# Optimization experiments

Measured on AMD Instinct MI355X. Metric: run time of the kernel, lower is better.

Reference implementation:

```python
import jax, jax.numpy as jnp
import numpy as np

TEMP = 2.0   # distillation temperature
KL_W = 0.2   # kl loss weight


def setup_inputs() -> dict:
    key = jax.random.key(0)
    ks = jax.random.split(key, 8)
    Ns, Nt, D, C = 16384, 16384, 64, 22
    return {
        "s_feat": jax.random.normal(ks[0], (Ns, D), dtype=jnp.float32),
        "t_feat": jax.random.normal(ks[1], (Nt, D), dtype=jnp.float32),
        "student_coords": jax.random.uniform(ks[2], (Ns, 3), dtype=jnp.float32),
        "teacher_coords": jax.random.uniform(ks[3], (Nt, 3), dtype=jnp.float32),
        "seg_W": jax.random.normal(ks[4], (C, D), dtype=jnp.float32) * 0.1,
        "seg_b": jnp.zeros((C,), jnp.float32),
        "seg_tW": jax.random.normal(ks[5], (C, D), dtype=jnp.float32) * 0.1,
        "seg_tb": jnp.zeros((C,), jnp.float32),
        "segment": jax.random.randint(ks[6], (Ns,), 0, C, dtype=jnp.int32),
    }


def reference(s_feat, t_feat, student_coords, teacher_coords,
              seg_W, seg_b, seg_tW, seg_tb, segment):
    Ns = s_feat.shape[0]
    # seg heads (Linear 64->22)
    seg_logits = s_feat @ seg_W.T + seg_b                      # [Ns, C]
    t_logits = jax.lax.stop_gradient(t_feat @ seg_tW.T + seg_tb)  # [Nt, C], teacher under no_grad

    # brute-force 1-NN: squared distances [Ns, Nt]
    d2 = (jnp.sum(student_coords ** 2, axis=1, keepdims=True)
          - 2.0 * student_coords @ teacher_coords.T
          + jnp.sum(teacher_coords ** 2, axis=1)[None, :])
    idx = jnp.argmin(d2, axis=1)                               # [Ns]
    matched = jax.lax.stop_gradient(t_logits[idx])             # gather teacher logits, k=1

    # KL distillation with temperature 2.0, reduction='batchmean', * T^2
    student_logp = jax.nn.log_softmax(seg_logits / TEMP, axis=1)
    teacher_p = jax.nn.softmax(matched / TEMP, axis=1)
    kl = jnp.sum(teacher_p * (jnp.log(teacher_p) - student_logp)) / Ns * (TEMP ** 2)
    kl_loss = KL_W * kl

    # cross-entropy seg loss
    logp = jax.nn.log_softmax(seg_logits, axis=1)
    seg_loss = -jnp.mean(jnp.take_along_axis(logp, segment[:, None], axis=1))

    total = seg_loss + kl_loss
    return jnp.stack([total, seg_loss, kl_loss])
```

## Files before the change

### kernel.cpp

```cpp
#include <hip/hip_runtime.h>
#include <math.h>

#define D 64
#define C 22
#define GRID 16
#define NCELL (GRID * GRID * GRID)
#define HCELL 0.0625f
#define TLP 24
#define TEMP_F 2.0f
#define KL_W_F 0.2f

__device__ __forceinline__ unsigned ord_of(float d) {
    unsigned b = __float_as_uint(d);
    return (b & 0x80000000u) ? ~b : (b | 0x80000000u);
}
__device__ __forceinline__ float bfly_max32(float v) {
#pragma unroll
    for (int off = 16; off; off >>= 1) v = fmaxf(v, __shfl_xor(v, off));
    return v;
}
__device__ __forceinline__ float bfly_sum32(float v) {
#pragma unroll
    for (int off = 16; off; off >>= 1) v += __shfl_xor(v, off);
    return v;
}
__device__ __forceinline__ unsigned long long bfly_min64(unsigned long long v) {
#pragma unroll
    for (int off = 32; off; off >>= 1) {
        unsigned long long o = __shfl_xor(v, off);
        v = (o < v) ? o : v;
    }
    return v;
}
__device__ __forceinline__ int cell_of(float x, float y, float z) {
    int cx = min(GRID - 1, (int)(x * GRID));
    int cy = min(GRID - 1, (int)(y * GRID));
    int cz = min(GRID - 1, (int)(z * GRID));
    return (cz * GRID + cy) * GRID + cx;
}

__device__ __forceinline__ void logits_role(
        const float* __restrict__ feat, const float* __restrict__ W,
        const float* __restrict__ bias, float* __restrict__ olog,
        float* smem, int row0, int N)
{
    float* w = smem;
    float* b = smem + C * D;
    for (int k = threadIdx.x; k < C * D; k += 256) w[k] = W[k];
    if (threadIdx.x < C) b[threadIdx.x] = bias[threadIdx.x];
    __syncthreads();

    int i = row0 + threadIdx.x;
    if (i >= N) return;

    float4 f[D / 4];
    const float4* fr = reinterpret_cast<const float4*>(feat + (size_t)i * D);
#pragma unroll
    for (int k = 0; k < D / 4; ++k) f[k] = fr[k];

    float* row = olog + (size_t)i * TLP;
#pragma unroll
    for (int c = 0; c < C; ++c) {
        float a = b[c];
        const float4* wr = reinterpret_cast<const float4*>(&w[c * D]);
#pragma unroll
        for (int k = 0; k < D / 4; ++k) {
            float4 wv = wr[k];
            a = fmaf(f[k].x, wv.x, a);
            a = fmaf(f[k].y, wv.y, a);
            a = fmaf(f[k].z, wv.z, a);
            a = fmaf(f[k].w, wv.w, a);
        }
        row[c] = a;
    }
}

__global__ void __launch_bounds__(256) build_kernel(
        const float* __restrict__ tc,
        const float* __restrict__ t_feat,
        const float* __restrict__ s_feat,
        const float* __restrict__ Wt, const float* __restrict__ bt,
        const float* __restrict__ Ws, const float* __restrict__ bs_,
        int*    __restrict__ head,
        float4* __restrict__ tc4,
        float*  __restrict__ tlog,
        float*  __restrict__ slog,
        float*  __restrict__ acc, unsigned* __restrict__ ct,
        int Ns, int Nt, int nlink, int ntb)
{
    __shared__ __align__(16) float smem[C * D + C];
    const int bx = blockIdx.x;

    if (bx == 0 && threadIdx.x == 0) { acc[0] = 0.f; acc[1] = 0.f; *ct = 0u; }

    if (bx < nlink) {
        int i = bx * 256 + threadIdx.x;
        if (i < Nt) {
            float x = tc[3 * i], y = tc[3 * i + 1], z = tc[3 * i + 2];
            int old = atomicExch(&head[cell_of(x, y, z)], i);
            tc4[i] = make_float4(x, y, z, __int_as_float(old));
        }
    } else if (bx < nlink + ntb) {
        logits_role(t_feat, Wt, bt, tlog, smem, (bx - nlink) * 256, Nt);
    } else {
        logits_role(s_feat, Ws, bs_, slog, smem, (bx - nlink - ntb) * 256, Ns);
    }
}

__global__ void __launch_bounds__(1024) main_kernel(
        const float* __restrict__ sc,
        const int*   __restrict__ segment,
        int*         __restrict__ head,
        const float4* __restrict__ tc4,
        const float* __restrict__ tlog,
        const float* __restrict__ slog,
        float* __restrict__ acc, unsigned* __restrict__ ct,
        float* __restrict__ out, int Ns, int Nt)
{
    __shared__ int ls_head[NCELL];
    __shared__ float rs[16], rk[16];
    __shared__ int lastF;
    if (threadIdx.x == 0) lastF = 0;
    for (int c = threadIdx.x; c < NCELL; c += 1024) ls_head[c] = head[c];
    __syncthreads();

    const int lane   = threadIdx.x & 63;
    const int wv     = threadIdx.x >> 6;
    const int nwaves = gridDim.x * 16;

    float seg_a = 0.f, kl_a = 0.f;

    for (int i = blockIdx.x * 16 + wv; i < Ns; i += nwaves) {
        float sx = sc[3 * i], sy = sc[3 * i + 1], sz = sc[3 * i + 2];
        const int scx = min(GRID - 1, (int)(sx * GRID));
        const int scy = min(GRID - 1, (int)(sy * GRID));
        const int scz = min(GRID - 1, (int)(sz * GRID));

        unsigned long long pk = ~0ULL;

        if (lane < 27) {
            int cx = scx + (lane % 3) - 1;
            int cy = scy + ((lane / 3) % 3) - 1;
            int cz = scz + (lane / 9) - 1;
            if (((unsigned)cx | (unsigned)cy | (unsigned)cz) < (unsigned)GRID) {
                int t = ls_head[(cz * GRID + cy) * GRID + cx];
                while ((unsigned)t < (unsigned)Nt) {
                    float4 q = tc4[t];
                    float ax = q.x - sx, ay = q.y - sy, az = q.z - sz;
                    float d2 = fmaf(ax, ax, fmaf(ay, ay, az * az));
                    unsigned long long cd =
                        ((unsigned long long)ord_of(d2) << 14)
                        | (unsigned long long)(unsigned)t;
                    if (cd < pk) pk = cd;
                    t = __float_as_int(q.w);
                }
            }
        }
        pk = bfly_min64(pk);
        unsigned mo = (unsigned)(pk >> 14);
        float bd2 = __uint_as_float((mo & 0x80000000u) ? (mo & 0x7FFFFFFFu) : ~mo);

        for (int r = 2; r <= GRID; ++r) {
            float rb = (float)(r - 1) * HCELL;
            if (bd2 <= rb * rb) break;
            int side = 2 * r + 1, nb = side * side * side;
            for (int b0 = 0; b0 < nb; b0 += 64) {
                int b = b0 + lane;
                if (b < nb) {
                    int dx = b % side - r;
                    int dy = (b / side) % side - r;
                    int dz = b / (side * side) - r;
                    int ch = max(abs(dx), max(abs(dy), abs(dz)));
                    int cx = scx + dx, cy = scy + dy, cz = scz + dz;
                    if (ch == r &&
                        (((unsigned)cx | (unsigned)cy | (unsigned)cz) < (unsigned)GRID)) {
                        int t = ls_head[(cz * GRID + cy) * GRID + cx];
                        while ((unsigned)t < (unsigned)Nt) {
                            float4 q = tc4[t];
                            float ax = q.x - sx, ay = q.y - sy, az = q.z - sz;
                            float d2 = fmaf(ax, ax, fmaf(ay, ay, az * az));
                            unsigned long long cd =
                                ((unsigned long long)ord_of(d2) << 14)
                                | (unsigned long long)(unsigned)t;
                            if (cd < pk) pk = cd;
                            t = __float_as_int(q.w);
                        }
                    }
                }
            }
            pk = bfly_min64(pk);
            mo = (unsigned)(pk >> 14);
            bd2 = __uint_as_float((mo & 0x80000000u) ? (mo & 0x7FFFFFFFu) : ~mo);
        }
        const int bidx = (int)(pk & 0x3FFFULL);

        const int half = lane >> 5;
        const int c    = lane & 31;
        float val = -INFINITY;
        if (c < C) val = half ? tlog[(size_t)bidx * TLP + c]
                              : slog[(size_t)i * TLP + c];
        float m  = bfly_max32(val);
        float dv = val - m;
        float dlc_u = __shfl(dv, c);

        float a0 = 0.f, a1 = 0.f;
        if (c < C) {
            if (half) {
                float u = expf(0.5f * dv);
                a0 = u;
                a1 = u * 0.5f * (dv - dlc_u);
            } else {
                a0 = expf(dv);
                a1 = expf(0.5f * dv);
            }
        }
        float s0 = bfly_sum32(a0);
        float s1 = bfly_sum32(a1);
        float U  = __shfl(s0, 32);
        float T  = __shfl(s1, 32);
        int   sg = segment[i];
        float lsg = __shfl(dv, sg);

        seg_a += logf(s0) - lsg;
        kl_a  += T / U + logf(s1) - logf(U);
    }

    if (lane == 0) { rs[wv] = seg_a; rk[wv] = kl_a; }
    __syncthreads();
    if (threadIdx.x == 0) {
        float s = 0.f, kk = 0.f;
#pragma unroll
        for (int w = 0; w < 16; ++w) { s += rs[w]; kk += rk[w]; }
        atomicAdd(&acc[0], s);
        atomicAdd(&acc[1], kk);
        __threadfence();
        unsigned t = atomicAdd(ct, 1u);
        if (t == gridDim.x - 1) lastF = 1;
    }
    __syncthreads();
    if (lastF) {
        for (int c = threadIdx.x; c < NCELL; c += 1024) head[c] = -1;
        if (threadIdx.x == 0) {
            float seg = atomicAdd(&acc[0], 0.f);
            float kl  = atomicAdd(&acc[1], 0.f);
            float seg_loss = seg / (float)Ns;
            float kl_loss  = KL_W_F * (kl / (float)Ns) * TEMP_F * TEMP_F;
            out[0] = seg_loss + kl_loss;
            out[1] = seg_loss;
            out[2] = kl_loss;
        }
    }
}

extern "C" void kernel_launch(void* const* d_in, const int* in_sizes, int n_in,
                              void* d_out, int out_size, void* d_ws, size_t ws_size,
                              hipStream_t stream)
{
    const float* s_feat  = (const float*)d_in[0];
    const float* t_feat  = (const float*)d_in[1];
    const float* s_coord = (const float*)d_in[2];
    const float* t_coord = (const float*)d_in[3];
    const float* seg_W   = (const float*)d_in[4];
    const float* seg_b   = (const float*)d_in[5];
    const float* seg_tW  = (const float*)d_in[6];
    const float* seg_tb  = (const float*)d_in[7];
    const int*   segment = (const int*)d_in[8];
    float* out = (float*)d_out;

    const int Ns = in_sizes[0] / D;
    const int Nt = in_sizes[1] / D;

    int*    head = (int*)d_ws;
    float4* tc4  = (float4*)(head + NCELL);
    float*  tlog = (float*)(tc4 + Nt);
    float*  slog = tlog + (size_t)Nt * TLP;
    float*  acc  = slog + (size_t)Ns * TLP;
    unsigned* ct = (unsigned*)(acc + 2);

    const int nlink = (Nt + 255) / 256;
    const int ntb   = (Nt + 255) / 256;
    const int nsb   = (Ns + 255) / 256;

    build_kernel<<<nlink + ntb + nsb, 256, 0, stream>>>(
        t_coord, t_feat, s_feat, seg_tW, seg_tb, seg_W, seg_b,
        head, tc4, tlog, slog, acc, ct, Ns, Nt, nlink, ntb);

    main_kernel<<<256, 1024, 0, stream>>>(
        s_coord, segment, head, tc4, tlog, slog, acc, ct, out, Ns, Nt);
}
```

Measured before the change: 48.65 us.

## Bin students into grid cells and share teacher neighbor scans across K students

Builds a student cell linked list alongside the teacher one and assigns one wave per grid cell. Each wave walks that cell's students in batches of K=8 and scans the 27 neighboring teacher cells once per batch, so each teacher point load is reused across up to eight students. The shared-memory copy of the head table is dropped and heads are read from global memory. Work per wave now depends on cell occupancy, which can leave waves unevenly loaded, and keeping eight 64-bit minima per lane raises register pressure.

```diff
diff --git a/kernel.cpp b/kernel.cpp
--- a/kernel.cpp
+++ b/kernel.cpp
@@ -7,6 +7,7 @@
 #define NCELL (GRID * GRID * GRID)
 #define HCELL 0.0625f
 #define TLP 24
+#define K 8
 #define TEMP_F 2.0f
 #define KL_W_F 0.2f
 
@@ -77,152 +78,190 @@
 
 __global__ void __launch_bounds__(256) build_kernel(
         const float* __restrict__ tc,
+        const float* __restrict__ sc,
         const float* __restrict__ t_feat,
         const float* __restrict__ s_feat,
         const float* __restrict__ Wt, const float* __restrict__ bt,
         const float* __restrict__ Ws, const float* __restrict__ bs_,
-        int*    __restrict__ head,
+        int*    __restrict__ head_t,
+        int*    __restrict__ head_s,
         float4* __restrict__ tc4,
-        float*  __restrict__ tlog,
-        float*  __restrict__ slog,
+        float4* __restrict__ sc4,
+        float*  __restrict__ tlog, float* __restrict__ slog,
         float*  __restrict__ acc, unsigned* __restrict__ ct,
-        int Ns, int Nt, int nlink, int ntb)
+        int Ns, int Nt, int nlt, int nls, int ntb)
 {
     __shared__ __align__(16) float smem[C * D + C];
     const int bx = blockIdx.x;
 
     if (bx == 0 && threadIdx.x == 0) { acc[0] = 0.f; acc[1] = 0.f; *ct = 0u; }
 
-    if (bx < nlink) {
+    if (bx < nlt) {
         int i = bx * 256 + threadIdx.x;
         if (i < Nt) {
             float x = tc[3 * i], y = tc[3 * i + 1], z = tc[3 * i + 2];
-            int old = atomicExch(&head[cell_of(x, y, z)], i);
+            int old = atomicExch(&head_t[cell_of(x, y, z)], i);
             tc4[i] = make_float4(x, y, z, __int_as_float(old));
         }
-    } else if (bx < nlink + ntb) {
-        logits_role(t_feat, Wt, bt, tlog, smem, (bx - nlink) * 256, Nt);
+    } else if (bx < nlt + nls) {
+        int i = (bx - nlt) * 256 + threadIdx.x;
+        if (i < Ns) {
+            float x = sc[3 * i], y = sc[3 * i + 1], z = sc[3 * i + 2];
+            int old = atomicExch(&head_s[cell_of(x, y, z)], i);
+            sc4[i] = make_float4(x, y, z, __int_as_float(old));
+        }
+    } else if (bx < nlt + nls + ntb) {
+        logits_role(t_feat, Wt, bt, tlog, smem, (bx - nlt - nls) * 256, Nt);
     } else {
-        logits_role(s_feat, Ws, bs_, slog, smem, (bx - nlink - ntb) * 256, Ns);
+        logits_role(s_feat, Ws, bs_, slog, smem, (bx - nlt - nls - ntb) * 256, Ns);
     }
 }
 
 __global__ void __launch_bounds__(1024) main_kernel(
-        const float* __restrict__ sc,
         const int*   __restrict__ segment,
-        int*         __restrict__ head,
+        int*         __restrict__ head_t,
+        int*         __restrict__ head_s,
         const float4* __restrict__ tc4,
+        const float4* __restrict__ sc4,
         const float* __restrict__ tlog,
         const float* __restrict__ slog,
         float* __restrict__ acc, unsigned* __restrict__ ct,
         float* __restrict__ out, int Ns, int Nt)
 {
-    __shared__ int ls_head[NCELL];
     __shared__ float rs[16], rk[16];
     __shared__ int lastF;
     if (threadIdx.x == 0) lastF = 0;
-    for (int c = threadIdx.x; c < NCELL; c += 1024) ls_head[c] = head[c];
-    __syncthreads();
-
-    const int lane   = threadIdx.x & 63;
-    const int wv     = threadIdx.x >> 6;
-    const int nwaves = gridDim.x * 16;
+
+    const int lane = threadIdx.x & 63;
+    const int wv   = threadIdx.x >> 6;
+    const int ci   = blockIdx.x * 16 + wv;
+    const int cx0  = ci & (GRID - 1);
+    const int cy0  = (ci >> 4) & (GRID - 1);
+    const int cz0  = ci >> 8;
 
     float seg_a = 0.f, kl_a = 0.f;
 
-    for (int i = blockIdx.x * 16 + wv; i < Ns; i += nwaves) {
-        float sx = sc[3 * i], sy = sc[3 * i + 1], sz = sc[3 * i + 2];
-        const int scx = min(GRID - 1, (int)(sx * GRID));
-        const int scy = min(GRID - 1, (int)(sy * GRID));
-        const int scz = min(GRID - 1, (int)(sz * GRID));
-
-        unsigned long long pk = ~0ULL;
+    int t = head_s[ci];
+    bool more = ((unsigned)t < (unsigned)Ns);
+
+    while (more) {
+        float sxx[K], syy[K], szz[K];
+        int   sid[K];
+        bool  sval[K];
+#pragma unroll
+        for (int k = 0; k < K; ++k) {
+            sval[k] = ((unsigned)t < (unsigned)Ns);
+            sid[k]  = t;
+            sxx[k] = 0.f; syy[k] = 0.f; szz[k] = 0.f;
+            if (sval[k]) {
+                float4 q = sc4[t];
+                sxx[k] = q.x; syy[k] = q.y; szz[k] = q.z;
+                t = __float_as_int(q.w);
+            }
+        }
+        more = ((unsigned)t < (unsigned)Ns);
+
+        unsigned long long pk[K];
+#pragma unroll
+        for (int k = 0; k < K; ++k) pk[k] = ~0ULL;
 
         if (lane < 27) {
-            int cx = scx + (lane % 3) - 1;
-            int cy = scy + ((lane / 3) % 3) - 1;
-            int cz = scz + (lane / 9) - 1;
+            int cx = cx0 + (lane % 3) - 1;
+            int cy = cy0 + ((lane / 3) % 3) - 1;
+            int cz = cz0 + (lane / 9) - 1;
             if (((unsigned)cx | (unsigned)cy | (unsigned)cz) < (unsigned)GRID) {
-                int t = ls_head[(cz * GRID + cy) * GRID + cx];
-                while ((unsigned)t < (unsigned)Nt) {
-                    float4 q = tc4[t];
-                    float ax = q.x - sx, ay = q.y - sy, az = q.z - sz;
-                    float d2 = fmaf(ax, ax, fmaf(ay, ay, az * az));
-                    unsigned long long cd =
-                        ((unsigned long long)ord_of(d2) << 14)
-                        | (unsigned long long)(unsigned)t;
-                    if (cd < pk) pk = cd;
-                    t = __float_as_int(q.w);
-                }
-            }
-        }
-        pk = bfly_min64(pk);
-        unsigned mo = (unsigned)(pk >> 14);
-        float bd2 = __uint_as_float((mo & 0x80000000u) ? (mo & 0x7FFFFFFFu) : ~mo);
-
-        for (int r = 2; r <= GRID; ++r) {
-            float rb = (float)(r - 1) * HCELL;
-            if (bd2 <= rb * rb) break;
-            int side = 2 * r + 1, nb = side * side * side;
-            for (int b0 = 0; b0 < nb; b0 += 64) {
-                int b = b0 + lane;
-                if (b < nb) {
-                    int dx = b % side - r;
-                    int dy = (b / side) % side - r;
-                    int dz = b / (side * side) - r;
-                    int ch = max(abs(dx), max(abs(dy), abs(dz)));
-                    int cx = scx + dx, cy = scy + dy, cz = scz + dz;
-                    if (ch == r &&
-                        (((unsigned)cx | (unsigned)cy | (unsigned)cz) < (unsigned)GRID)) {
-                        int t = ls_head[(cz * GRID + cy) * GRID + cx];
-                        while ((unsigned)t < (unsigned)Nt) {
-                            float4 q = tc4[t];
-                            float ax = q.x - sx, ay = q.y - sy, az = q.z - sz;
+                int tt = head_t[(cz * GRID + cy) * GRID + cx];
+                while ((unsigned)tt < (unsigned)Nt) {
+                    float4 q = tc4[tt];
+#pragma unroll
+                    for (int k = 0; k < K; ++k) {
+                        if (sval[k]) {
+                            float ax = q.x - sxx[k], ay = q.y - syy[k], az = q.z - szz[k];
                             float d2 = fmaf(ax, ax, fmaf(ay, ay, az * az));
                             unsigned long long cd =
                                 ((unsigned long long)ord_of(d2) << 14)
-                                | (unsigned long long)(unsigned)t;
-                            if (cd < pk) pk = cd;
-                            t = __float_as_int(q.w);
+                                | (unsigned long long)(unsigned)tt;
+                            if (cd < pk[k]) pk[k] = cd;
+                        }
+                    }
+                    tt = __float_as_int(q.w);
+                }
+            }
+        }
+#pragma unroll
+        for (int k = 0; k < K; ++k) pk[k] = bfly_min64(pk[k]);
+
+#pragma unroll
+        for (int k = 0; k < K; ++k) {
+            if (!sval[k]) continue;
+
+            unsigned mo = (unsigned)(pk[k] >> 14);
+            float bd2 = __uint_as_float((mo & 0x80000000u) ? (mo & 0x7FFFFFFFu) : ~mo);
+            for (int r = 2; r <= GRID; ++r) {
+                float rb = (float)(r - 1) * HCELL;
+                if (bd2 <= rb * rb) break;
+                int side = 2 * r + 1, nb = side * side * side;
+                for (int b0 = 0; b0 < nb; b0 += 64) {
+                    int b = b0 + lane;
+                    if (b < nb) {
+                        int dx = b % side - r;
+                        int dy = (b / side) % side - r;
+                        int dz = b / (side * side) - r;
+                        int ch = max(abs(dx), max(abs(dy), abs(dz)));
+                        int cx = cx0 + dx, cy = cy0 + dy, cz = cz0 + dz;
+                        if (ch == r &&
+                            (((unsigned)cx | (unsigned)cy | (unsigned)cz) < (unsigned)GRID)) {
+                            int tt = head_t[(cz * GRID + cy) * GRID + cx];
+                            while ((unsigned)tt < (unsigned)Nt) {
+                                float4 q = tc4[tt];
+                                float ax = q.x - sxx[k], ay = q.y - syy[k], az = q.z - szz[k];
+                                float d2 = fmaf(ax, ax, fmaf(ay, ay, az * az));
+                                unsigned long long cd =
+                                    ((unsigned long long)ord_of(d2) << 14)
+                                    | (unsigned long long)(unsigned)tt;
+                                if (cd < pk[k]) pk[k] = cd;
+                                tt = __float_as_int(q.w);
+                            }
                         }
                     }
                 }
+                pk[k] = bfly_min64(pk[k]);
+                mo  = (unsigned)(pk[k] >> 14);
+                bd2 = __uint_as_float((mo & 0x80000000u) ? (mo & 0x7FFFFFFFu) : ~mo);
             }
-            pk = bfly_min64(pk);
-            mo = (unsigned)(pk >> 14);
-            bd2 = __uint_as_float((mo & 0x80000000u) ? (mo & 0x7FFFFFFFu) : ~mo);
-        }
-        const int bidx = (int)(pk & 0x3FFFULL);
-
-        const int half = lane >> 5;
-        const int c    = lane & 31;
-        float val = -INFINITY;
-        if (c < C) val = half ? tlog[(size_t)bidx * TLP + c]
-                              : slog[(size_t)i * TLP + c];
-        float m  = bfly_max32(val);
-        float dv = val - m;
-        float dlc_u = __shfl(dv, c);
-
-        float a0 = 0.f, a1 = 0.f;
-        if (c < C) {
-            if (half) {
-                float u = expf(0.5f * dv);
-                a0 = u;
-                a1 = u * 0.5f * (dv - dlc_u);
-            } else {
-                a0 = expf(dv);
-                a1 = expf(0.5f * dv);
+            const int bidx = (int)(pk[k] & 0x3FFFULL);
+            const int i    = sid[k];
+
+            const int half = lane >> 5;
+            const int c    = lane & 31;
+            float val = -INFINITY;
+            if (c < C) val = half ? tlog[(size_t)bidx * TLP + c]
+                                  : slog[(size_t)i * TLP + c];
+            float m  = bfly_max32(val);
+            float dv = val - m;
+            float dlc_u = __shfl(dv, c);
+
+            float a0 = 0.f, a1 = 0.f;
+            if (c < C) {
+                if (half) {
+                    float u = expf(0.5f * dv);
+                    a0 = u;
+                    a1 = u * 0.5f * (dv - dlc_u);
+                } else {
+                    a0 = expf(dv);
+                    a1 = expf(0.5f * dv);
+                }
             }
-        }
-        float s0 = bfly_sum32(a0);
-        float s1 = bfly_sum32(a1);
-        float U  = __shfl(s0, 32);
-        float T  = __shfl(s1, 32);
-        int   sg = segment[i];
-        float lsg = __shfl(dv, sg);
-
-        seg_a += logf(s0) - lsg;
-        kl_a  += T / U + logf(s1) - logf(U);
+            float s0 = bfly_sum32(a0);
+            float s1 = bfly_sum32(a1);
+            float U  = __shfl(s0, 32);
+            float T  = __shfl(s1, 32);
+            int   sg = segment[i];
+            float lsg = __shfl(dv, sg);
+
+            seg_a += logf(s0) - lsg;
+            kl_a  += T / U + logf(s1) - logf(U);
+        }
     }
 
     if (lane == 0) { rs[wv] = seg_a; rk[wv] = kl_a; }
@@ -234,12 +273,12 @@
         atomicAdd(&acc[0], s);
         atomicAdd(&acc[1], kk);
         __threadfence();
-        unsigned t = atomicAdd(ct, 1u);
-        if (t == gridDim.x - 1) lastF = 1;
+        unsigned tk = atomicAdd(ct, 1u);
+        if (tk == gridDim.x - 1) lastF = 1;
     }
     __syncthreads();
     if (lastF) {
-        for (int c = threadIdx.x; c < NCELL; c += 1024) head[c] = -1;
+        for (int c = threadIdx.x; c < NCELL; c += 1024) { head_t[c] = -1; head_s[c] = -1; }
         if (threadIdx.x == 0) {
             float seg = atomicAdd(&acc[0], 0.f);
             float kl  = atomicAdd(&acc[1], 0.f);
@@ -270,21 +309,24 @@
     const int Ns = in_sizes[0] / D;
     const int Nt = in_sizes[1] / D;
 
-    int*    head = (int*)d_ws;
-    float4* tc4  = (float4*)(head + NCELL);
-    float*  tlog = (float*)(tc4 + Nt);
-    float*  slog = tlog + (size_t)Nt * TLP;
-    float*  acc  = slog + (size_t)Ns * TLP;
-    unsigned* ct = (unsigned*)(acc + 2);
-
-    const int nlink = (Nt + 255) / 256;
-    const int ntb   = (Nt + 255) / 256;
-    const int nsb   = (Ns + 255) / 256;
-
-    build_kernel<<<nlink + ntb + nsb, 256, 0, stream>>>(
-        t_coord, t_feat, s_feat, seg_tW, seg_tb, seg_W, seg_b,
-        head, tc4, tlog, slog, acc, ct, Ns, Nt, nlink, ntb);
-
-    main_kernel<<<256, 1024, 0, stream>>>(
-        s_coord, segment, head, tc4, tlog, slog, acc, ct, out, Ns, Nt);
-}
+    int*    head_t = (int*)d_ws;
+    int*    head_s = head_t + NCELL;
+    float4* tc4    = (float4*)(head_s + NCELL);
+    float4* sc4    = tc4 + Nt;
+    float*  tlog   = (float*)(sc4 + Ns);
+    float*  slog   = tlog + (size_t)Nt * TLP;
+    float*  acc    = slog + (size_t)Ns * TLP;
+    unsigned* ct   = (unsigned*)(acc + 2);
+
+    const int nlt = (Nt + 255) / 256;
+    const int nls = (Ns + 255) / 256;
+    const int ntb = (Nt + 255) / 256;
+    const int nsb = (Ns + 255) / 256;
+
+    build_kernel<<<nlt + nls + ntb + nsb, 256, 0, stream>>>(
+        t_coord, s_coord, t_feat, s_feat, seg_tW, seg_tb, seg_W, seg_b,
+        head_t, head_s, tc4, sc4, tlog, slog, acc, ct, Ns, Nt, nlt, nls, ntb);
+
+    main_kernel<<<(NCELL + 15) / 16, 1024, 0, stream>>>(
+        segment, head_t, head_s, tc4, sc4, tlog, slog, acc, ct, out, Ns, Nt);
+}
```

Measured after the change: 55.30 us. 1.14x slower.
